# Performance work log

Hardware: AMD Instinct MI355X
Metric: run time of the kernel (lower is better)

## Reference

```python
import jax, jax.numpy as jnp
import numpy as np

# Production-scale dims: ViT patch attention on a 32x32 patch grid
B, L, F = 16, 1024, 512      # batch, seq (=NX*NY patches), model dim
H, D = 8, 64                 # heads, head_dim (F = H*D)
NX, NY = 32, 32              # patch grid; Toeplitz table size 4*NX*NY = 4096


def setup_inputs() -> dict:
    key = jax.random.key(0)
    ks = jax.random.split(key, 12)
    w = lambda k, shp: jax.random.normal(k, shp, jnp.float32) * 0.02
    return {
        "inputs_q": jax.random.normal(ks[0], (B, L, F), jnp.float32),
        "inputs_kv": jax.random.normal(ks[1], (B, L, F), jnp.float32),
        "Wq": w(ks[2], (F, H * D)), "bq": jnp.zeros((H * D,), jnp.float32),
        "Wk": w(ks[3], (F, H * D)), "bk": jnp.zeros((H * D,), jnp.float32),
        "Wv": w(ks[4], (F, H * D)), "bv": jnp.zeros((H * D,), jnp.float32),
        "Wo": w(ks[5], (H * D, F)), "bo": jnp.zeros((F,), jnp.float32),
        "toeplitz": w(ks[6], (H, 4 * NX * NY)),
    }


def _rel_index():
    # 2D relative-position (Toeplitz) index: patch p -> (x, y) on NX x NY grid.
    coords = jnp.arange(L)
    xi, yi = coords // NY, coords % NY
    dx = xi[:, None] - xi[None, :] + NX          # in [1, 2*NX-1]
    dy = yi[:, None] - yi[None, :] + NY          # in [1, 2*NY-1]
    return dx * (2 * NY) + dy                    # [L, L] indices into 4*NX*NY table


def reference(inputs_q, inputs_kv, Wq, bq, Wk, bk, Wv, bv, Wo, bo, toeplitz):
    q = (inputs_q @ Wq + bq).reshape(B, L, H, D)
    k = (inputs_kv @ Wk + bk).reshape(B, L, H, D)
    v = (inputs_kv @ Wv + bv).reshape(B, L, H, D)
    bias = toeplitz[:, _rel_index()]             # [H, L, L] Toeplitz relative bias
    scale = 1.0 / jnp.sqrt(jnp.float32(D))
    scores = jnp.einsum("bqhd,bkhd->bhqk", q, k) * scale + bias  # [B,H,L,L]
    attn = jax.nn.softmax(scores, axis=-1)
    x = jnp.einsum("bhqk,bkhd->bqhd", attn, v).reshape(B, L, H * D)
    out = x @ Wo + bo
    return out.reshape(B, L, H, D)               # matches torch forward's final reshape
```

## Files before the change

### kernel.cpp

```cpp
#include <hip/hip_runtime.h>
#include <hip/hip_bf16.h>

#define B_  16
#define L_  1024
#define F_  512
#define H_  8
#define D_  64
#define M_  (B_ * L_)
#define HD_ 512

typedef __bf16 bf16x8 __attribute__((ext_vector_type(8)));
typedef __bf16 bf16x4 __attribute__((ext_vector_type(4)));
typedef short  s16x4  __attribute__((ext_vector_type(4)));
typedef float  f32x4  __attribute__((ext_vector_type(4)));

__device__ __forceinline__ void gl_lds16(const void* g, void* l) {
  __builtin_amdgcn_global_load_lds(
      (const __attribute__((address_space(1))) unsigned int*)g,
      (__attribute__((address_space(3))) unsigned int*)l, 16, 0, 0);
}

__global__ __launch_bounds__(256) void wt_kernel(
    const float* __restrict__ Wq, const float* __restrict__ Wk,
    const float* __restrict__ Wv, const float* __restrict__ Wo,
    __bf16* __restrict__ Wt_all)
{
  const float* W = (blockIdx.z == 0) ? Wq : (blockIdx.z == 1) ? Wk
                 : (blockIdx.z == 2) ? Wv : Wo;
  __bf16* Wt = Wt_all + (size_t)blockIdx.z * (512 * 512);
  __shared__ float s[32][33];
  const int t = threadIdx.x;
  const int r = t >> 5, c = t & 31;
  const int k0 = blockIdx.x * 32, n0 = blockIdx.y * 32;
#pragma unroll
  for (int i = 0; i < 4; ++i)
    s[r + i * 8][c] = W[(size_t)(k0 + r + i * 8) * 512 + n0 + c];
  __syncthreads();
#pragma unroll
  for (int i = 0; i < 4; ++i)
    Wt[(size_t)(n0 + r + i * 8) * 512 + k0 + c] = (__bf16)s[c][r + i * 8];
}

__global__ __launch_bounds__(256) void gemm_proj_kernel(
    const float* __restrict__ Xq, const float* __restrict__ Xkv,
    const __bf16* __restrict__ Wt_all,
    const float* __restrict__ bq, const float* __restrict__ bk_,
    const float* __restrict__ bv_,
    __bf16* __restrict__ qd, __bf16* __restrict__ kd, __bf16* __restrict__ vd,
    int ybase)
{
  const int by = blockIdx.y + ybase;
  const int seg = by >> 2;
  const float* X = (seg == 0) ? Xq : Xkv;
  const __bf16* Wt = Wt_all + (size_t)seg * 262144;
  const float* bias = (seg == 0) ? bq : (seg == 1) ? bk_ : bv_;
  __bf16* dst = (seg == 0) ? qd : (seg == 1) ? kd : vd;
  const int mode = seg;

  __shared__ __align__(16) __bf16 As[2][4][128][8];
  __shared__ __align__(16) __bf16 Bs[2][4][128][8];
  const int t = threadIdx.x;
  const int m0 = blockIdx.x * 128, n0 = (by & 3) * 128;
  const int lane = t & 63, w = t >> 6;
  const int ml = lane & 15, quad = lane >> 4;
  const int wm = w & 1, wn = w >> 1;

  f32x4 acc[4][4];
#pragma unroll
  for (int i = 0; i < 4; ++i)
#pragma unroll
    for (int j = 0; j < 4; ++j) acc[i][j] = (f32x4){0.f, 0.f, 0.f, 0.f};

  const int ako0 = t & 3,          arow0 = t >> 2;
  const int ako1 = (t + 256) & 3,  arow1 = (t + 256) >> 2;
  const int bs0 = w * 64 + lane,   bs1 = (w + 4) * 64 + lane;
  const int bko0 = bs0 >> 7, brow0 = bs0 & 127;
  const int bko1 = bs1 >> 7, brow1 = bs1 & 127;

  float4 fa0, fa1, fa2, fa3;

#define ALOAD(kk)                                                               \
  do {                                                                          \
    const float* p0 = X + (size_t)(m0 + arow0) * 512 + (kk) + ako0 * 8;         \
    const float* p1 = X + (size_t)(m0 + arow1) * 512 + (kk) + ako1 * 8;         \
    fa0 = *(const float4*)p0; fa1 = *(const float4*)(p0 + 4);                   \
    fa2 = *(const float4*)p1; fa3 = *(const float4*)(p1 + 4);                   \
  } while (0)

#define AWRITE(buf)                                                             \
  do {                                                                          \
    bf16x8 v0, v1;                                                              \
    v0[0] = (__bf16)fa0.x; v0[1] = (__bf16)fa0.y; v0[2] = (__bf16)fa0.z;        \
    v0[3] = (__bf16)fa0.w; v0[4] = (__bf16)fa1.x; v0[5] = (__bf16)fa1.y;        \
    v0[6] = (__bf16)fa1.z; v0[7] = (__bf16)fa1.w;                               \
    v1[0] = (__bf16)fa2.x; v1[1] = (__bf16)fa2.y; v1[2] = (__bf16)fa2.z;        \
    v1[3] = (__bf16)fa2.w; v1[4] = (__bf16)fa3.x; v1[5] = (__bf16)fa3.y;        \
    v1[6] = (__bf16)fa3.z; v1[7] = (__bf16)fa3.w;                               \
    *(bf16x8*)&As[buf][ako0][arow0][0] = v0;                                    \
    *(bf16x8*)&As[buf][ako1][arow1][0] = v1;                                    \
  } while (0)

#define BSTAGE(buf, kk)                                                         \
  do {                                                                          \
    gl_lds16(&Wt[(size_t)(n0 + brow0) * 512 + (kk) + bko0 * 8],                 \
             &Bs[buf][bko0][brow0][0]);                                         \
    gl_lds16(&Wt[(size_t)(n0 + brow1) * 512 + (kk) + bko1 * 8],                 \
             &Bs[buf][bko1][brow1][0]);                                         \
  } while (0)

#define COMPUTE_TILE(buf)                                                       \
  do {                                                                          \
    bf16x8 a[4], b[4];                                                          \
    _Pragma("unroll") for (int mt = 0; mt < 4; ++mt)                            \
        a[mt] = *(const bf16x8*)&As[buf][quad][wm * 64 + mt * 16 + ml][0];      \
    _Pragma("unroll") for (int nt = 0; nt < 4; ++nt)                            \
        b[nt] = *(const bf16x8*)&Bs[buf][quad][wn * 64 + nt * 16 + ml][0];      \
    _Pragma("unroll") for (int mt = 0; mt < 4; ++mt)                            \
        _Pragma("unroll") for (int nt = 0; nt < 4; ++nt)                        \
            acc[mt][nt] = __builtin_amdgcn_mfma_f32_16x16x32_bf16(              \
                a[mt], b[nt], acc[mt][nt], 0, 0, 0);                            \
  } while (0)

  BSTAGE(0, 0);
  ALOAD(0);
  AWRITE(0);
  __syncthreads();

#pragma unroll
  for (int tt = 0; tt < 15; ++tt) {
    const int cur = tt & 1, nxt = cur ^ 1;
    ALOAD((tt + 1) * 32);
    BSTAGE(nxt, (tt + 1) * 32);
    COMPUTE_TILE(cur);
    AWRITE(nxt);
    __syncthreads();
  }
  COMPUTE_TILE(1);

#pragma unroll
  for (int nt = 0; nt < 4; ++nt) {
    int col = n0 + wn * 64 + nt * 16 + ml;
    float bv = bias[col];
    int h = col >> 6, d = col & 63;
#pragma unroll
    for (int mt = 0; mt < 4; ++mt) {
      int row0 = m0 + wm * 64 + mt * 16 + quad * 4;
      int bz = row0 >> 10;
      int l0 = row0 & 1023;
      if (mode == 2) {
        bf16x4 pk;
#pragma unroll
        for (int r = 0; r < 4; ++r) pk[r] = (__bf16)(acc[mt][nt][r] + bv);
        size_t idx = ((size_t)(bz * H_ + h) * D_ + d) * L_ + l0;
        *(bf16x4*)&dst[idx] = pk;
      } else {
        size_t base = ((size_t)(bz * H_ + h) * L_ + l0) * D_ + d;
#pragma unroll
        for (int r = 0; r < 4; ++r)
          dst[base + (size_t)r * D_] = (__bf16)(acc[mt][nt][r] + bv);
      }
    }
  }
#undef ALOAD
#undef AWRITE
#undef BSTAGE
#undef COMPUTE_TILE
}

__global__ __launch_bounds__(256, 2) void attn_kernel(
    const __bf16* __restrict__ qg,
    const __bf16* __restrict__ kg,
    const __bf16* __restrict__ vg,
    const float* __restrict__ toep_g,
    __bf16* __restrict__ xg)
{
  __shared__ float toep[4096];
  __shared__ __align__(16) __bf16 Ks[2][64][64];
  __shared__ __align__(16) __bf16 Vs[2][64][64];

  const int t = threadIdx.x;
  const int n = blockIdx.x;
  const int bh = ((n >> 5) << 3) | (n & 7);
  const int q0 = ((n >> 3) & 3) * 256;
  const int h = bh & 7;
  const int lane = t & 63, w = t >> 6;
  const int ml = lane & 15, quad = lane >> 4;
  const int lo3 = lane >> 3;
  const int kop = lane & 7;

  const size_t qkbase = (size_t)bh * (L_ * D_);
  const size_t vbase  = (size_t)bh * (D_ * L_);

  {
    const float4* src = (const float4*)(toep_g + (size_t)h * 4096);
    float4* dl = (float4*)toep;
    for (int i = t; i < 1024; i += 256) dl[i] = src[i];
  }

#pragma unroll
  for (int i = 0; i < 2; ++i) {
    int row = (w * 2 + i) * 8 + lo3;
    int ko = kop ^ lo3;
    gl_lds16(&kg[qkbase + (size_t)row * D_ + ko * 8], &Ks[0][row][kop * 8]);
    gl_lds16(&vg[vbase + (size_t)row * L_ + ko * 8], &Vs[0][row][kop * 8]);
  }

  bf16x8 qf[4][2];
#pragma unroll
  for (int qn = 0; qn < 4; ++qn) {
    const __bf16* qp =
        qg + qkbase + (size_t)(q0 + w * 64 + qn * 16 + ml) * D_ + quad * 8;
    qf[qn][0] = *(const bf16x8*)qp;
    qf[qn][1] = *(const bf16x8*)(qp + 32);
  }

  float lpart[4] = {0.f, 0.f, 0.f, 0.f};
  f32x4 o[4][4];
#pragma unroll
  for (int qn = 0; qn < 4; ++qn)
#pragma unroll
    for (int dt = 0; dt < 4; ++dt) o[qn][dt] = (f32x4){0.f, 0.f, 0.f, 0.f};

  __syncthreads();

  int cur = 0;
  for (int k0 = 0; k0 < L_; k0 += 64) {
    if (k0 + 64 < L_) {
      int nb = cur ^ 1;
#pragma unroll
      for (int i = 0; i < 2; ++i) {
        int row = (w * 2 + i) * 8 + lo3;
        int ko = kop ^ lo3;
        gl_lds16(&kg[qkbase + (size_t)(k0 + 64 + row) * D_ + ko * 8],
                 &Ks[nb][row][kop * 8]);
        gl_lds16(&vg[vbase + (size_t)row * L_ + k0 + 64 + ko * 8],
                 &Vs[nb][row][kop * 8]);
      }
    }

    const int cb0 = (((q0 + w * 64) >> 5) - (k0 >> 5) + 31) * 64 +
                    (ml - quad * 4 + 16);
    float tc[3][3][4];
#pragma unroll
    for (int a = 0; a < 3; ++a)
#pragma unroll
      for (int b = 0; b < 3; ++b) {
        const int cb = cb0 + a * 64 + b * 16;
#pragma unroll
        for (int r = 0; r < 4; ++r) tc[a][b][r] = toep[cb - r];
      }

#pragma unroll
    for (int nt = 0; nt < 4; ++nt) {
      bf16x8 kf0 = *(const bf16x8*)&Ks[cur][nt * 16 + ml][(quad ^ (ml & 7)) * 8];
      bf16x8 kf1 =
          *(const bf16x8*)&Ks[cur][nt * 16 + ml][((4 + quad) ^ (ml & 7)) * 8];

      s16x4 pfrag[4];
#pragma unroll
      for (int qn = 0; qn < 4; ++qn) {
        f32x4 z = (f32x4){0.f, 0.f, 0.f, 0.f};
        z = __builtin_amdgcn_mfma_f32_16x16x32_bf16(kf0, qf[qn][0], z, 0, 0, 0);
        z = __builtin_amdgcn_mfma_f32_16x16x32_bf16(kf1, qf[qn][1], z, 0, 0, 0);

        float p[4];
#pragma unroll
        for (int r = 0; r < 4; ++r)
          p[r] = __expf(fmaf(z[r], 0.125f,
                             tc[(qn >> 1) - (nt >> 1) + 1]
                               [(qn & 1) - (nt & 1) + 1][r]));
        lpart[qn] += (p[0] + p[1]) + (p[2] + p[3]);
        bf16x4 pk;
#pragma unroll
        for (int r = 0; r < 4; ++r) pk[r] = (__bf16)p[r];
        pfrag[qn] = __builtin_bit_cast(s16x4, pk);
      }

#pragma unroll
      for (int dt = 0; dt < 4; ++dt) {
        int row = dt * 16 + ml;
        int gc = nt * 2 + (quad >> 1);
        bf16x4 vfr = *(const bf16x4*)
            &Vs[cur][row][((gc ^ (row & 7)) * 8) + (quad & 1) * 4];
        s16x4 vfs = __builtin_bit_cast(s16x4, vfr);
#pragma unroll
        for (int qn = 0; qn < 4; ++qn)
          o[qn][dt] = __builtin_amdgcn_mfma_f32_16x16x16bf16_1k(
              pfrag[qn], vfs, o[qn][dt], 0, 0, 0);
      }
    }

    __syncthreads();
    cur ^= 1;
  }

#pragma unroll
  for (int qn = 0; qn < 4; ++qn) {
    lpart[qn] += __shfl_xor(lpart[qn], 16);
    lpart[qn] += __shfl_xor(lpart[qn], 32);
  }
  float linv[4][4];
#pragma unroll
  for (int qn = 0; qn < 4; ++qn)
#pragma unroll
    for (int r = 0; r < 4; ++r)
      linv[qn][r] = 1.0f / __shfl(lpart[qn], quad * 16 + quad * 4 + r);

#pragma unroll
  for (int qn = 0; qn < 4; ++qn)
#pragma unroll
    for (int dt = 0; dt < 4; ++dt)
#pragma unroll
      for (int r = 0; r < 4; ++r) {
        int row = q0 + w * 64 + qn * 16 + quad * 4 + r;
        xg[((size_t)(bh >> 3) * L_ + row) * 512 + h * 64 + dt * 16 + ml] =
            (__bf16)(o[qn][dt][r] * linv[qn][r]);
      }
}

__global__ __launch_bounds__(256, 4) void gemm_out_kernel(
    const __bf16* __restrict__ Xb,
    const __bf16* __restrict__ Wt,
    const float* __restrict__ bo,
    float* __restrict__ out)
{
  __shared__ __align__(16) __bf16 As[2][4][128][8];
  __shared__ __align__(16) __bf16 Bs[2][4][128][8];
  const int t = threadIdx.x;
  const int m0 = blockIdx.x * 128, n0 = blockIdx.y * 128;
  const int lane = t & 63, w = t >> 6;
  const int ml = lane & 15, quad = lane >> 4;
  const int wm = w & 1, wn = w >> 1;

  f32x4 acc[4][4];
#pragma unroll
  for (int i = 0; i < 4; ++i)
#pragma unroll
    for (int j = 0; j < 4; ++j) acc[i][j] = (f32x4){0.f, 0.f, 0.f, 0.f};

  const int slot0 = w * 64 + lane;
  const int slot1 = (w + 4) * 64 + lane;
  const int ko0 = slot0 >> 7, row0_ = slot0 & 127;
  const int ko1 = slot1 >> 7, row1_ = slot1 & 127;

#define STAGE_OUT(buf, kk)                                                      \
  do {                                                                          \
    gl_lds16(&Xb[(size_t)(m0 + row0_) * 512 + (kk) + ko0 * 8],                  \
             &As[buf][ko0][row0_][0]);                                          \
    gl_lds16(&Wt[(size_t)(n0 + row0_) * 512 + (kk) + ko0 * 8],                  \
             &Bs[buf][ko0][row0_][0]);                                          \
    gl_lds16(&Xb[(size_t)(m0 + row1_) * 512 + (kk) + ko1 * 8],                  \
             &As[buf][ko1][row1_][0]);                                          \
    gl_lds16(&Wt[(size_t)(n0 + row1_) * 512 + (kk) + ko1 * 8],                  \
             &Bs[buf][ko1][row1_][0]);                                          \
  } while (0)

#define COMPUTE_TILE_O(buf)                                                     \
  do {                                                                          \
    bf16x8 a[4], b[4];                                                          \
    _Pragma("unroll") for (int mt = 0; mt < 4; ++mt)                            \
        a[mt] = *(const bf16x8*)&As[buf][quad][wm * 64 + mt * 16 + ml][0];      \
    _Pragma("unroll") for (int nt = 0; nt < 4; ++nt)                            \
        b[nt] = *(const bf16x8*)&Bs[buf][quad][wn * 64 + nt * 16 + ml][0];      \
    _Pragma("unroll") for (int mt = 0; mt < 4; ++mt)                            \
        _Pragma("unroll") for (int nt = 0; nt < 4; ++nt)                        \
            acc[mt][nt] = __builtin_amdgcn_mfma_f32_16x16x32_bf16(              \
                a[mt], b[nt], acc[mt][nt], 0, 0, 0);                            \
  } while (0)

  STAGE_OUT(0, 0);
#pragma unroll
  for (int tt = 0; tt < 15; ++tt) {
    const int cur = tt & 1;
    STAGE_OUT(cur ^ 1, (tt + 1) * 32);
    asm volatile("s_waitcnt vmcnt(4)" ::: "memory");
    asm volatile("s_barrier" ::: "memory");
    COMPUTE_TILE_O(cur);
    asm volatile("s_barrier" ::: "memory");
  }
  asm volatile("s_waitcnt vmcnt(0)" ::: "memory");
  asm volatile("s_barrier" ::: "memory");
  COMPUTE_TILE_O(1);

#pragma unroll
  for (int nt = 0; nt < 4; ++nt) {
    int col = n0 + wn * 64 + nt * 16 + ml;
    float bv = bo[col];
#pragma unroll
    for (int mt = 0; mt < 4; ++mt) {
      int row0 = m0 + wm * 64 + mt * 16 + quad * 4;
#pragma unroll
      for (int r = 0; r < 4; ++r)
        out[(size_t)(row0 + r) * 512 + col] = acc[mt][nt][r] + bv;
    }
  }
#undef STAGE_OUT
#undef COMPUTE_TILE_O
}

extern "C" void kernel_launch(void* const* d_in, const int* in_sizes, int n_in,
                              void* d_out, int out_size, void* d_ws, size_t ws_size,
                              hipStream_t stream) {
  const float* inputs_q  = (const float*)d_in[0];
  const float* inputs_kv = (const float*)d_in[1];
  const float* Wq = (const float*)d_in[2];
  const float* bq = (const float*)d_in[3];
  const float* Wk = (const float*)d_in[4];
  const float* bk = (const float*)d_in[5];
  const float* Wv = (const float*)d_in[6];
  const float* bv = (const float*)d_in[7];
  const float* Wo = (const float*)d_in[8];
  const float* bo = (const float*)d_in[9];
  const float* toep = (const float*)d_in[10];
  float* out = (float*)d_out;

  char* ws = (char*)d_ws;
  __bf16* qb  = (__bf16*)(ws);
  __bf16* kb  = (__bf16*)(ws + 16777216);
  __bf16* vb  = (__bf16*)(ws + 33554432);
  __bf16* xb  = (__bf16*)(ws + 50331648);
  __bf16* Wt  = (__bf16*)(ws + 67108864);

  wt_kernel<<<dim3(16, 16, 4), 256, 0, stream>>>(Wq, Wk, Wv, Wo, Wt);
  gemm_proj_kernel<<<dim3(128, 6), 256, 0, stream>>>(
      inputs_q, inputs_kv, Wt, bq, bk, bv, qb, kb, vb, 0);
  gemm_proj_kernel<<<dim3(128, 6), 256, 0, stream>>>(
      inputs_q, inputs_kv, Wt, bq, bk, bv, qb, kb, vb, 6);
  attn_kernel<<<dim3(512), 256, 0, stream>>>(qb, kb, vb, toep, xb);
  gemm_out_kernel<<<dim3(128, 4), 256, 0, stream>>>(xb, Wt + 3 * 262144, bo, out);
}
```

Measured before the change: 262.4 us.

## Fold softmax scale into Q, use exp2, MFMA row sums, triple-buffer GEMMs

The Q projection epilogue now multiplies by scale*log2e and the Toeplitz table is pre-scaled by log2e, so the attention inner loop can call the raw v_exp_f32 instruction in place of __expf with an fma. Softmax row sums are now accumulated with an MFMA against a ones vector, which removes the scalar adds and the cross-lane shuffles. Both projection and output GEMMs move to a three-stage B (and A in the output GEMM) LDS ring with explicit waitcnt and barrier control. The two projection launches are merged into one, and gemm_out's occupancy hint drops from 4 to 2 to fit the larger LDS. Risks include extra MFMA pressure in attention, lower occupancy in gemm_out, and small precision shifts from the fast exp.

```diff
diff --git a/kernel.cpp b/kernel.cpp
--- a/kernel.cpp
+++ b/kernel.cpp
@@ -19,6 +19,19 @@
       (const __attribute__((address_space(1))) unsigned int*)g,
       (__attribute__((address_space(3))) unsigned int*)l, 16, 0, 0);
 }
+
+__device__ __forceinline__ float exp2_fast(float x) {
+  float r;
+  asm("v_exp_f32 %0, %1" : "=v"(r) : "v"(x));
+  return r;
+}
+
+#define WAIT_VM_LG(N)                                                           \
+  asm volatile("s_waitcnt vmcnt(" #N ") lgkmcnt(0)" ::: "memory")
+#define BARRIER() asm volatile("s_barrier" ::: "memory")
+
+#define QSCALE 0.18033688f
+#define LOG2E  1.44269504f
 
 __global__ __launch_bounds__(256) void wt_kernel(
     const float* __restrict__ Wq, const float* __restrict__ Wk,
@@ -46,19 +59,19 @@
     const __bf16* __restrict__ Wt_all,
     const float* __restrict__ bq, const float* __restrict__ bk_,
     const float* __restrict__ bv_,
-    __bf16* __restrict__ qd, __bf16* __restrict__ kd, __bf16* __restrict__ vd,
-    int ybase)
+    __bf16* __restrict__ qd, __bf16* __restrict__ kd, __bf16* __restrict__ vd)
 {
-  const int by = blockIdx.y + ybase;
+  const int by = blockIdx.y;
   const int seg = by >> 2;
   const float* X = (seg == 0) ? Xq : Xkv;
   const __bf16* Wt = Wt_all + (size_t)seg * 262144;
   const float* bias = (seg == 0) ? bq : (seg == 1) ? bk_ : bv_;
   __bf16* dst = (seg == 0) ? qd : (seg == 1) ? kd : vd;
   const int mode = seg;
+  const float oscale = (seg == 0) ? QSCALE : 1.0f;
 
   __shared__ __align__(16) __bf16 As[2][4][128][8];
-  __shared__ __align__(16) __bf16 Bs[2][4][128][8];
+  __shared__ __align__(16) __bf16 Bs[3][4][128][8];
   const int t = threadIdx.x;
   const int m0 = blockIdx.x * 128, n0 = (by & 3) * 128;
   const int lane = t & 63, w = t >> 6;
@@ -108,34 +121,45 @@
              &Bs[buf][bko1][brow1][0]);                                         \
   } while (0)
 
-#define COMPUTE_TILE(buf)                                                       \
+#define COMPUTE_TILE(ab, bb)                                                    \
   do {                                                                          \
     bf16x8 a[4], b[4];                                                          \
     _Pragma("unroll") for (int mt = 0; mt < 4; ++mt)                            \
-        a[mt] = *(const bf16x8*)&As[buf][quad][wm * 64 + mt * 16 + ml][0];      \
+        a[mt] = *(const bf16x8*)&As[ab][quad][wm * 64 + mt * 16 + ml][0];       \
     _Pragma("unroll") for (int nt = 0; nt < 4; ++nt)                            \
-        b[nt] = *(const bf16x8*)&Bs[buf][quad][wn * 64 + nt * 16 + ml][0];      \
+        b[nt] = *(const bf16x8*)&Bs[bb][quad][wn * 64 + nt * 16 + ml][0];       \
     _Pragma("unroll") for (int mt = 0; mt < 4; ++mt)                            \
         _Pragma("unroll") for (int nt = 0; nt < 4; ++nt)                        \
             acc[mt][nt] = __builtin_amdgcn_mfma_f32_16x16x32_bf16(              \
                 a[mt], b[nt], acc[mt][nt], 0, 0, 0);                            \
   } while (0)
 
+  ALOAD(0);
   BSTAGE(0, 0);
-  ALOAD(0);
+  BSTAGE(1, 32);
   AWRITE(0);
-  __syncthreads();
-
-#pragma unroll
-  for (int tt = 0; tt < 15; ++tt) {
-    const int cur = tt & 1, nxt = cur ^ 1;
-    ALOAD((tt + 1) * 32);
-    BSTAGE(nxt, (tt + 1) * 32);
-    COMPUTE_TILE(cur);
-    AWRITE(nxt);
-    __syncthreads();
-  }
-  COMPUTE_TILE(1);
+  WAIT_VM_LG(2);
+  BARRIER();
+
+  int bcur = 0, bst = 2;
+  for (int tt = 0; tt < 16; ++tt) {
+    if (tt < 15) ALOAD((tt + 1) * 32);
+    if (tt < 14) BSTAGE(bst, (tt + 2) * 32);
+    COMPUTE_TILE(tt & 1, bcur);
+    if (tt < 14) {
+      WAIT_VM_LG(2);
+      AWRITE((tt + 1) & 1);
+      asm volatile("s_waitcnt lgkmcnt(0)" ::: "memory");
+      BARRIER();
+    } else if (tt == 14) {
+      WAIT_VM_LG(0);
+      AWRITE((tt + 1) & 1);
+      asm volatile("s_waitcnt lgkmcnt(0)" ::: "memory");
+      BARRIER();
+    }
+    bcur = (bcur == 2) ? 0 : bcur + 1;
+    bst = (bst == 2) ? 0 : bst + 1;
+  }
 
 #pragma unroll
   for (int nt = 0; nt < 4; ++nt) {
@@ -157,7 +181,7 @@
         size_t base = ((size_t)(bz * H_ + h) * L_ + l0) * D_ + d;
 #pragma unroll
         for (int r = 0; r < 4; ++r)
-          dst[base + (size_t)r * D_] = (__bf16)(acc[mt][nt][r] + bv);
+          dst[base + (size_t)r * D_] = (__bf16)((acc[mt][nt][r] + bv) * oscale);
       }
     }
   }
@@ -194,7 +218,11 @@
   {
     const float4* src = (const float4*)(toep_g + (size_t)h * 4096);
     float4* dl = (float4*)toep;
-    for (int i = t; i < 1024; i += 256) dl[i] = src[i];
+    for (int i = t; i < 1024; i += 256) {
+      float4 v = src[i];
+      v.x *= LOG2E; v.y *= LOG2E; v.z *= LOG2E; v.w *= LOG2E;
+      dl[i] = v;
+    }
   }
 
 #pragma unroll
@@ -214,12 +242,16 @@
     qf[qn][1] = *(const bf16x8*)(qp + 32);
   }
 
-  float lpart[4] = {0.f, 0.f, 0.f, 0.f};
+  const s16x4 ones = {(short)0x3F80, (short)0x3F80, (short)0x3F80, (short)0x3F80};
+
+  f32x4 acc_l[4];
   f32x4 o[4][4];
 #pragma unroll
-  for (int qn = 0; qn < 4; ++qn)
+  for (int qn = 0; qn < 4; ++qn) {
+    acc_l[qn] = (f32x4){0.f, 0.f, 0.f, 0.f};
 #pragma unroll
     for (int dt = 0; dt < 4; ++dt) o[qn][dt] = (f32x4){0.f, 0.f, 0.f, 0.f};
+  }
 
   __syncthreads();
 
@@ -266,14 +298,14 @@
         float p[4];
 #pragma unroll
         for (int r = 0; r < 4; ++r)
-          p[r] = __expf(fmaf(z[r], 0.125f,
-                             tc[(qn >> 1) - (nt >> 1) + 1]
-                               [(qn & 1) - (nt & 1) + 1][r]));
-        lpart[qn] += (p[0] + p[1]) + (p[2] + p[3]);
+          p[r] = exp2_fast(z[r] + tc[(qn >> 1) - (nt >> 1) + 1]
+                                    [(qn & 1) - (nt & 1) + 1][r]);
         bf16x4 pk;
 #pragma unroll
         for (int r = 0; r < 4; ++r) pk[r] = (__bf16)p[r];
         pfrag[qn] = __builtin_bit_cast(s16x4, pk);
+        acc_l[qn] = __builtin_amdgcn_mfma_f32_16x16x16bf16_1k(
+            pfrag[qn], ones, acc_l[qn], 0, 0, 0);
       }
 
 #pragma unroll
@@ -294,17 +326,12 @@
     cur ^= 1;
   }
 
-#pragma unroll
-  for (int qn = 0; qn < 4; ++qn) {
-    lpart[qn] += __shfl_xor(lpart[qn], 16);
-    lpart[qn] += __shfl_xor(lpart[qn], 32);
-  }
   float linv[4][4];
 #pragma unroll
   for (int qn = 0; qn < 4; ++qn)
 #pragma unroll
     for (int r = 0; r < 4; ++r)
-      linv[qn][r] = 1.0f / __shfl(lpart[qn], quad * 16 + quad * 4 + r);
+      linv[qn][r] = 1.0f / acc_l[qn][r];
 
 #pragma unroll
   for (int qn = 0; qn < 4; ++qn)
@@ -318,14 +345,14 @@
       }
 }
 
-__global__ __launch_bounds__(256, 4) void gemm_out_kernel(
+__global__ __launch_bounds__(256, 2) void gemm_out_kernel(
     const __bf16* __restrict__ Xb,
     const __bf16* __restrict__ Wt,
     const float* __restrict__ bo,
     float* __restrict__ out)
 {
-  __shared__ __align__(16) __bf16 As[2][4][128][8];
-  __shared__ __align__(16) __bf16 Bs[2][4][128][8];
+  __shared__ __align__(16) __bf16 As[3][4][128][8];
+  __shared__ __align__(16) __bf16 Bs[3][4][128][8];
   const int t = threadIdx.x;
   const int m0 = blockIdx.x * 128, n0 = blockIdx.y * 128;
   const int lane = t & 63, w = t >> 6;
@@ -369,18 +396,20 @@
   } while (0)
 
   STAGE_OUT(0, 0);
-#pragma unroll
+  STAGE_OUT(1, 32);
+
+  int bcur = 0, bst = 2;
   for (int tt = 0; tt < 15; ++tt) {
-    const int cur = tt & 1;
-    STAGE_OUT(cur ^ 1, (tt + 1) * 32);
-    asm volatile("s_waitcnt vmcnt(4)" ::: "memory");
-    asm volatile("s_barrier" ::: "memory");
-    COMPUTE_TILE_O(cur);
-    asm volatile("s_barrier" ::: "memory");
-  }
-  asm volatile("s_waitcnt vmcnt(0)" ::: "memory");
-  asm volatile("s_barrier" ::: "memory");
-  COMPUTE_TILE_O(1);
+    WAIT_VM_LG(4);
+    BARRIER();
+    if (tt < 14) STAGE_OUT(bst, (tt + 2) * 32);
+    COMPUTE_TILE_O(bcur);
+    bcur = (bcur == 2) ? 0 : bcur + 1;
+    bst = (bst == 2) ? 0 : bst + 1;
+  }
+  WAIT_VM_LG(0);
+  BARRIER();
+  COMPUTE_TILE_O(bcur);
 
 #pragma unroll
   for (int nt = 0; nt < 4; ++nt) {
@@ -422,10 +451,8 @@
   __bf16* Wt  = (__bf16*)(ws + 67108864);
 
   wt_kernel<<<dim3(16, 16, 4), 256, 0, stream>>>(Wq, Wk, Wv, Wo, Wt);
-  gemm_proj_kernel<<<dim3(128, 6), 256, 0, stream>>>(
-      inputs_q, inputs_kv, Wt, bq, bk, bv, qb, kb, vb, 0);
-  gemm_proj_kernel<<<dim3(128, 6), 256, 0, stream>>>(
-      inputs_q, inputs_kv, Wt, bq, bk, bv, qb, kb, vb, 6);
+  gemm_proj_kernel<<<dim3(128, 12), 256, 0, stream>>>(
+      inputs_q, inputs_kv, Wt, bq, bk, bv, qb, kb, vb);
   attn_kernel<<<dim3(512), 256, 0, stream>>>(qb, kb, vb, toep, xb);
   gemm_out_kernel<<<dim3(128, 4), 256, 0, stream>>>(xb, Wt + 3 * 262144, bo, out);
 }
```

Measured after the change: 258.5 us. Within noise of the previous version (-1.5%).
